# Optimization experiments

Hardware: AMD Instinct MI355X
Metric: run time of the kernel (lower is better)

## Reference

```python
import jax, jax.numpy as jnp
import numpy as np

N = 50000          # nodes
E = 800000         # edges (avg degree 16)
NS = 0.01          # LeakyReLU negative slope
N_CONVS = 3


def setup_inputs() -> dict:
    key = jax.random.key(0)
    ks = jax.random.split(key, 12)
    g = lambda k, s: (jax.random.normal(k, s, dtype=jnp.float32) * 0.05)
    return dict(
        x=jax.random.normal(ks[0], (N, 16), dtype=jnp.float32),
        edge_index=jax.random.randint(ks[1], (2, E), 0, N),
        edge_weight=jax.random.uniform(ks[2], (E, 1), dtype=jnp.float32),
        # prep MLP: Linear(16,64)+LeakyReLU, Linear(64,64)+Tanh
        Wp_in=g(ks[3], (16, 64)), bp_in=jnp.zeros((64,), jnp.float32),
        Wp_h=g(ks[4], (64, 64)), bp_h=jnp.zeros((64,), jnp.float32),
        # per-conv edge projection Linear(edge_dim=1, 64), stacked over 3 convs
        We=g(ks[5], (N_CONVS, 1, 64)), be=jnp.zeros((N_CONVS, 64), jnp.float32),
        # per-conv nn MLP: Linear(64,64)+LeakyReLU, Linear(64,64)+Tanh
        Wm0=g(ks[6], (N_CONVS, 64, 64)), bm0=jnp.zeros((N_CONVS, 64), jnp.float32),
        Wm1=g(ks[7], (N_CONVS, 64, 64)), bm1=jnp.zeros((N_CONVS, 64), jnp.float32),
        # post MLP: Linear(64,64)+LeakyReLU, Linear(64,32)+Tanh
        Wq0=g(ks[8], (64, 64)), bq0=jnp.zeros((64,), jnp.float32),
        Wq1=g(ks[9], (64, 32)), bq1=jnp.zeros((32,), jnp.float32),
    )


def reference(x, edge_index, edge_weight,
              Wp_in, bp_in, Wp_h, bp_h,
              We, be, Wm0, bm0, Wm1, bm1,
              Wq0, bq0, Wq1, bq1):
    lrelu = lambda v: jax.nn.leaky_relu(v, NS)
    # prep MLP (dropout=0 -> no-op)
    h = lrelu(x @ Wp_in + bp_in)
    h = jnp.tanh(h @ Wp_h + bp_h)
    src, dst = edge_index[0], edge_index[1]
    # stacked GINEConv layers (eps=0): out = nn(x + sum_j ReLU(x_j + lin_e(e_ij)))
    for k in range(N_CONVS):
        e = edge_weight @ We[k] + be[k]              # [E,64] edge embedding
        msg = jax.nn.relu(h[src] + e)                # [E,64] gather + fuse
        agg = jax.ops.segment_sum(msg, dst, num_segments=N)  # [N,64] scatter-sum
        z = agg + h                                  # (1+eps)*x with eps=0
        z = lrelu(z @ Wm0[k] + bm0[k])
        h = jnp.tanh(z @ Wm1[k] + bm1[k])
    # post MLP
    z = lrelu(h @ Wq0 + bq0)
    return jnp.tanh(z @ Wq1 + bq1)                   # [N,32]
```

## Files before the change

kernel.cpp:

```cpp
#include <hip/hip_runtime.h>
#include <hip/hip_fp16.h>
#include <math.h>

#define NS 0.01f
#define CAP 48
#define QS (1.f / 65535.f)

__device__ __forceinline__ float lrelu(float v) { return fmaxf(v, NS * v); }

__global__ void __launch_bounds__(512) build_kernel(
    const int* __restrict__ src, const int* __restrict__ dst,
    const float* __restrict__ ew, int* __restrict__ cnt,
    unsigned* __restrict__ bucket, int E, int fillBlocks,
    const float* __restrict__ x,
    const float* __restrict__ Wp_in, const float* __restrict__ bp_in,
    const float* __restrict__ Wp_h,  const float* __restrict__ bp_h,
    __half* __restrict__ h, int N, int prepBlocks,
    const float* __restrict__ Wm0, const float* __restrict__ Wm1,
    const float* __restrict__ Wq0, const float* __restrict__ Wq1,
    float* __restrict__ WT)
{
    __shared__ float zt[64 * 65];
    const int b = (int)blockIdx.x;
    const int t = threadIdx.x;

    if (b < fillBlocks) {
        const int e = b * 512 + t;
        if (e < E) {
            const int d = dst[e];
            const int p = atomicAdd(&cnt[d], 1);
            if (p < CAP) {
                const unsigned q = __float2uint_rn(ew[e] * 65535.f) & 0xffffu;
                bucket[(size_t)d * CAP + p] = ((unsigned)src[e] << 16) | q;
            }
        }
        return;
    }
    if (b < fillBlocks + prepBlocks) {
        const int n0 = (b - fillBlocks) * 64;
        #pragma unroll
        for (int r = 0; r < 2; ++r) {
            const int idx = r * 512 + t;
            const int nl = idx >> 4, i = idx & 15;
            const int n = n0 + nl;
            zt[nl * 65 + i] = (n < N) ? x[(size_t)n * 16 + i] : 0.f;
        }
        __syncthreads();
        const int lane = t & 63;
        const int w = __builtin_amdgcn_readfirstlane(t >> 6);
        float zx[16];
        #pragma unroll
        for (int i = 0; i < 16; ++i) zx[i] = zt[lane * 65 + i];
        float y[8];
        #pragma unroll
        for (int jj = 0; jj < 8; ++jj) {
            const int j = w * 8 + jj;
            float a = bp_in[j];
            #pragma unroll
            for (int i = 0; i < 16; ++i) a = fmaf(zx[i], Wp_in[i * 64 + j], a);
            y[jj] = lrelu(a);
        }
        __syncthreads();
        #pragma unroll
        for (int jj = 0; jj < 8; ++jj) zt[lane * 65 + w * 8 + jj] = y[jj];
        __syncthreads();
        #pragma unroll
        for (int jj = 0; jj < 8; ++jj) y[jj] = bp_h[w * 8 + jj];
        #pragma unroll
        for (int half = 0; half < 2; ++half) {
            float zh[32];
            #pragma unroll
            for (int i = 0; i < 32; ++i) zh[i] = zt[lane * 65 + half * 32 + i];
            #pragma unroll
            for (int jj = 0; jj < 8; ++jj) {
                const int j = w * 8 + jj;
                #pragma unroll
                for (int i = 0; i < 32; ++i)
                    y[jj] = fmaf(zh[i], Wp_h[(half * 32 + i) * 64 + j], y[jj]);
            }
        }
        __syncthreads();
        #pragma unroll
        for (int jj = 0; jj < 8; ++jj) zt[lane * 65 + w * 8 + jj] = tanhf(y[jj]);
        __syncthreads();
        #pragma unroll
        for (int r = 0; r < 8; ++r) {
            const int idx = r * 512 + t;
            const int nl = idx >> 6, i = idx & 63;
            const int n = n0 + nl;
            if (n < N) h[(size_t)n * 64 + i] = __float2half(zt[nl * 65 + i]);
        }
        return;
    }
    const int o = (b - fillBlocks - prepBlocks) * 512 + t;
    if (o >= 30720) return;
    float v;
    int d = o;
    if (d < 12288) {
        const int k = d >> 12, r = d & 4095, j = r >> 6, i = r & 63;
        v = Wm0[k * 4096 + i * 64 + j];
    } else if ((d -= 12288) < 12288) {
        const int k = d >> 12, r = d & 4095, j = r >> 6, i = r & 63;
        v = Wm1[k * 4096 + i * 64 + j];
    } else if ((d -= 12288) < 4096) {
        const int j = d >> 6, i = d & 63;
        v = Wq0[i * 64 + j];
    } else {
        d -= 4096;
        const int j = d >> 6, i = d & 63;
        v = Wq1[i * 32 + j];
    }
    WT[o] = v;
}

__device__ __forceinline__ void drain_edges(float& acc, int p, int len,
    const unsigned* row,
    const __half* __restrict__ hin, int lane, float wej, float bej)
{
    if (p + 4 <= len) {
        const uint4 a = ((const uint4*)row)[p >> 2];
        const unsigned r[4] = {a.x, a.y, a.z, a.w};
        float g[4];
        #pragma unroll
        for (int q = 0; q < 4; ++q) g[q] = __half2float(hin[(size_t)(r[q] >> 16) * 64 + lane]);
        #pragma unroll
        for (int q = 0; q < 4; ++q)
            acc += fmaxf(g[q] + fmaf((float)(r[q] & 0xffffu) * QS, wej, bej), 0.f);
        p += 4;
    }
    for (; p < len; ++p) {
        const unsigned r = row[p];
        acc += fmaxf(__half2float(hin[(size_t)(r >> 16) * 64 + lane])
                     + fmaf((float)(r & 0xffffu) * QS, wej, bej), 0.f);
    }
}

__device__ __forceinline__ void layer64s(float* zt, int lane, int w,
                                         const float* __restrict__ WT,
                                         const float* __restrict__ bias, int act)
{
    float y[4];
    #pragma unroll
    for (int jj = 0; jj < 4; ++jj) y[jj] = bias[w * 4 + jj];
    #pragma unroll
    for (int half = 0; half < 2; ++half) {
        float zh[32];
        #pragma unroll
        for (int i = 0; i < 32; ++i) zh[i] = zt[lane * 65 + half * 32 + i];
        #pragma unroll
        for (int jj = 0; jj < 4; ++jj) {
            const float* wr = WT + (w * 4 + jj) * 64 + half * 32;
            #pragma unroll
            for (int i = 0; i < 32; ++i) y[jj] = fmaf(zh[i], wr[i], y[jj]);
        }
    }
    __syncthreads();
    #pragma unroll
    for (int jj = 0; jj < 4; ++jj)
        zt[lane * 65 + w * 4 + jj] = act ? lrelu(y[jj]) : tanhf(y[jj]);
    __syncthreads();
}

__global__ void __launch_bounds__(1024, 8) fused_conv_kernel(
    const __half* __restrict__ hin,
    const int* __restrict__ cnt,
    const unsigned* __restrict__ bucket,
    const float* __restrict__ We_k, const float* __restrict__ be_k,
    const float* __restrict__ W0T, const float* __restrict__ b0,
    const float* __restrict__ W1T, const float* __restrict__ b1,
    const float* __restrict__ Wq0T, const float* __restrict__ bq0,
    const float* __restrict__ Wq1T, const float* __restrict__ bq1,
    int do_post, __half* __restrict__ hout, float* __restrict__ out, int N)
{
    __shared__ float zt[64 * 65];
    const int t = threadIdx.x;
    const int lane = t & 63;
    const int w = __builtin_amdgcn_readfirstlane(t >> 6);
    const int n0 = (int)blockIdx.x * 64;
    const float wej = We_k[lane], bej = be_k[lane];

    float acc[4];
    int   len[4];
    const unsigned* row[4];
    #pragma unroll
    for (int s = 0; s < 4; ++s) {
        const int n = n0 + w * 4 + s;
        if (n < N) { acc[s] = __half2float(hin[(size_t)n * 64 + lane]); len[s] = min(cnt[n], CAP); }
        else       { acc[s] = 0.f; len[s] = 0; }
        row[s] = bucket + (size_t)n * CAP;
    }
    const int maxLen = max(max(len[0], len[1]), max(len[2], len[3]));
    for (int p = 0; p + 8 <= maxLen; p += 8) {
        #pragma unroll
        for (int s = 0; s < 4; ++s) {
            if (p + 8 <= len[s]) {
                const uint4* r4 = (const uint4*)row[s];
                const uint4 a0 = r4[p >> 2], a1 = r4[(p >> 2) + 1];
                const unsigned rr[8] = {a0.x, a0.y, a0.z, a0.w, a1.x, a1.y, a1.z, a1.w};
                float g[8];
                #pragma unroll
                for (int q = 0; q < 8; ++q)
                    g[q] = __half2float(hin[(size_t)(rr[q] >> 16) * 64 + lane]);
                #pragma unroll
                for (int q = 0; q < 8; ++q)
                    acc[s] += fmaxf(g[q] + fmaf((float)(rr[q] & 0xffffu) * QS, wej, bej), 0.f);
            }
        }
    }
    #pragma unroll
    for (int s = 0; s < 4; ++s) {
        drain_edges(acc[s], len[s] & ~7, len[s], row[s], hin, lane, wej, bej);
        zt[(w * 4 + s) * 65 + lane] = acc[s];
    }
    __syncthreads();

    layer64s(zt, lane, w, W0T, b0, 1);
    layer64s(zt, lane, w, W1T, b1, 0);

    if (!do_post) {
        #pragma unroll
        for (int r = 0; r < 4; ++r) {
            const int idx = r * 1024 + t;
            const int nl = idx >> 6, i = idx & 63;
            const int n = n0 + nl;
            if (n < N) hout[(size_t)n * 64 + i] = __float2half(zt[nl * 65 + i]);
        }
        return;
    }
    layer64s(zt, lane, w, Wq0T, bq0, 1);
    {
        float y[2];
        #pragma unroll
        for (int jj = 0; jj < 2; ++jj) y[jj] = bq1[w * 2 + jj];
        #pragma unroll
        for (int half = 0; half < 2; ++half) {
            float zh[32];
            #pragma unroll
            for (int i = 0; i < 32; ++i) zh[i] = zt[lane * 65 + half * 32 + i];
            #pragma unroll
            for (int jj = 0; jj < 2; ++jj) {
                const float* wr = Wq1T + (w * 2 + jj) * 64 + half * 32;
                #pragma unroll
                for (int i = 0; i < 32; ++i) y[jj] = fmaf(zh[i], wr[i], y[jj]);
            }
        }
        __syncthreads();
        #pragma unroll
        for (int jj = 0; jj < 2; ++jj) zt[lane * 65 + w * 2 + jj] = tanhf(y[jj]);
        __syncthreads();
    }
    #pragma unroll
    for (int r = 0; r < 2; ++r) {
        const int idx = r * 1024 + t;
        const int nl = idx >> 5, i = idx & 31;
        const int n = n0 + nl;
        if (n < N) out[(size_t)n * 32 + i] = zt[nl * 65 + i];
    }
}

extern "C" void kernel_launch(void* const* d_in, const int* in_sizes, int n_in,
                              void* d_out, int out_size, void* d_ws, size_t ws_size,
                              hipStream_t stream) {
    const float* x     = (const float*)d_in[0];
    const int*   ei    = (const int*)d_in[1];
    const float* ew    = (const float*)d_in[2];
    const float* Wp_in = (const float*)d_in[3];
    const float* bp_in = (const float*)d_in[4];
    const float* Wp_h  = (const float*)d_in[5];
    const float* bp_h  = (const float*)d_in[6];
    const float* We    = (const float*)d_in[7];
    const float* be    = (const float*)d_in[8];
    const float* Wm0   = (const float*)d_in[9];
    const float* bm0   = (const float*)d_in[10];
    const float* Wm1   = (const float*)d_in[11];
    const float* bm1   = (const float*)d_in[12];
    const float* Wq0   = (const float*)d_in[13];
    const float* bq0   = (const float*)d_in[14];
    const float* Wq1   = (const float*)d_in[15];
    const float* bq1   = (const float*)d_in[16];
    float* out = (float*)d_out;

    const int N = in_sizes[0] / 16;
    const int E = in_sizes[2];
    const int* src = ei;
    const int* dst = ei + E;

    __half*   hA     = (__half*)d_ws;
    __half*   hB     = hA + (size_t)N * 64;
    unsigned* bucket = (unsigned*)(hB + (size_t)N * 64);
    int*      cnt    = (int*)(bucket + (size_t)N * CAP);
    float*    WT     = (float*)(cnt + N);
    float* Wm0T   = WT;
    float* Wm1T   = Wm0T + 12288;
    float* Wq0T   = Wm1T + 12288;
    float* Wq1T   = Wq0T + 4096;

    const int fillBlocks = (E + 511) / 512;
    const int prepBlocks = (N + 63) / 64;
    const int wtBlocks   = (30720 + 511) / 512;
    const int tileBlocks = (N + 63) / 64;

    hipMemsetAsync(cnt, 0, (size_t)N * sizeof(int), stream);
    build_kernel<<<fillBlocks + prepBlocks + wtBlocks, 512, 0, stream>>>(
        src, dst, ew, cnt, bucket, E, fillBlocks,
        x, Wp_in, bp_in, Wp_h, bp_h, hA, N, prepBlocks,
        Wm0, Wm1, Wq0, Wq1, WT);

    fused_conv_kernel<<<tileBlocks, 1024, 0, stream>>>(
        hA, cnt, bucket, We + 0 * 64, be + 0 * 64,
        Wm0T + 0 * 4096, bm0 + 0 * 64, Wm1T + 0 * 4096, bm1 + 0 * 64,
        Wq0T, bq0, Wq1T, bq1, 0, hB, out, N);
    fused_conv_kernel<<<tileBlocks, 1024, 0, stream>>>(
        hB, cnt, bucket, We + 1 * 64, be + 1 * 64,
        Wm0T + 1 * 4096, bm0 + 1 * 64, Wm1T + 1 * 4096, bm1 + 1 * 64,
        Wq0T, bq0, Wq1T, bq1, 0, hA, out, N);
    fused_conv_kernel<<<tileBlocks, 1024, 0, stream>>>(
        hA, cnt, bucket, We + 2 * 64, be + 2 * 64,
        Wm0T + 2 * 4096, bm0 + 2 * 64, Wm1T + 2 * 4096, bm1 + 2 * 64,
        Wq0T, bq0, Wq1T, bq1, 1, hB, out, N);
}
```

Baseline: 298.5 us.

## Fuse three conv launches into one persistent cooperative kernel with grid sync

Replaces the three per-layer conv kernel launches with a single cooperative persistent kernel. It loops over layers, processes node tiles in a grid-stride loop, and separates layers with a grid-wide sync while swapping the ping-pong buffers. The goal is to remove launch gaps and per-launch tail effects. In exchange it adds grid-sync overhead and an occupancy-limited grid size (hard-coded for 256 CUs), and each block must now loop over several tiles.

```diff
diff --git a/kernel.cpp b/kernel.cpp
--- a/kernel.cpp
+++ b/kernel.cpp
@@ -1,6 +1,9 @@
 #include <hip/hip_runtime.h>
+#include <hip/hip_cooperative_groups.h>
 #include <hip/hip_fp16.h>
 #include <math.h>
+
+namespace cg = cooperative_groups;
 
 #define NS 0.01f
 #define CAP 48
@@ -161,100 +164,118 @@
     __syncthreads();
 }
 
-__global__ void __launch_bounds__(1024, 8) fused_conv_kernel(
-    const __half* __restrict__ hin,
+__global__ void __launch_bounds__(1024, 8) conv3_kernel(
+    __half* __restrict__ hA, __half* __restrict__ hB,
     const int* __restrict__ cnt,
     const unsigned* __restrict__ bucket,
-    const float* __restrict__ We_k, const float* __restrict__ be_k,
-    const float* __restrict__ W0T, const float* __restrict__ b0,
-    const float* __restrict__ W1T, const float* __restrict__ b1,
+    const float* __restrict__ We, const float* __restrict__ be,
+    const float* __restrict__ Wm0T, const float* __restrict__ bm0,
+    const float* __restrict__ Wm1T, const float* __restrict__ bm1,
     const float* __restrict__ Wq0T, const float* __restrict__ bq0,
     const float* __restrict__ Wq1T, const float* __restrict__ bq1,
-    int do_post, __half* __restrict__ hout, float* __restrict__ out, int N)
+    float* __restrict__ out, int N, int tiles)
 {
+    cg::grid_group gridg = cg::this_grid();
     __shared__ float zt[64 * 65];
     const int t = threadIdx.x;
     const int lane = t & 63;
     const int w = __builtin_amdgcn_readfirstlane(t >> 6);
-    const int n0 = (int)blockIdx.x * 64;
-    const float wej = We_k[lane], bej = be_k[lane];
-
-    float acc[4];
-    int   len[4];
-    const unsigned* row[4];
-    #pragma unroll
-    for (int s = 0; s < 4; ++s) {
-        const int n = n0 + w * 4 + s;
-        if (n < N) { acc[s] = __half2float(hin[(size_t)n * 64 + lane]); len[s] = min(cnt[n], CAP); }
-        else       { acc[s] = 0.f; len[s] = 0; }
-        row[s] = bucket + (size_t)n * CAP;
-    }
-    const int maxLen = max(max(len[0], len[1]), max(len[2], len[3]));
-    for (int p = 0; p + 8 <= maxLen; p += 8) {
-        #pragma unroll
-        for (int s = 0; s < 4; ++s) {
-            if (p + 8 <= len[s]) {
-                const uint4* r4 = (const uint4*)row[s];
-                const uint4 a0 = r4[p >> 2], a1 = r4[(p >> 2) + 1];
-                const unsigned rr[8] = {a0.x, a0.y, a0.z, a0.w, a1.x, a1.y, a1.z, a1.w};
-                float g[8];
+
+    const __half* hin = hA;
+    __half* hout = hB;
+    for (int k = 0; k < 3; ++k) {
+        const float wej = We[k * 64 + lane], bej = be[k * 64 + lane];
+        const float* W0T = Wm0T + k * 4096; const float* b0 = bm0 + k * 64;
+        const float* W1T = Wm1T + k * 4096; const float* b1 = bm1 + k * 64;
+        const int do_post = (k == 2);
+
+        for (int tile = (int)blockIdx.x; tile < tiles; tile += (int)gridDim.x) {
+            const int n0 = tile * 64;
+
+            float acc[4];
+            int   len[4];
+            const unsigned* row[4];
+            #pragma unroll
+            for (int s = 0; s < 4; ++s) {
+                const int n = n0 + w * 4 + s;
+                if (n < N) { acc[s] = __half2float(hin[(size_t)n * 64 + lane]); len[s] = min(cnt[n], CAP); }
+                else       { acc[s] = 0.f; len[s] = 0; }
+                row[s] = bucket + (size_t)n * CAP;
+            }
+            const int maxLen = max(max(len[0], len[1]), max(len[2], len[3]));
+            for (int p = 0; p + 8 <= maxLen; p += 8) {
                 #pragma unroll
-                for (int q = 0; q < 8; ++q)
-                    g[q] = __half2float(hin[(size_t)(rr[q] >> 16) * 64 + lane]);
+                for (int s = 0; s < 4; ++s) {
+                    if (p + 8 <= len[s]) {
+                        const uint4* r4 = (const uint4*)row[s];
+                        const uint4 a0 = r4[p >> 2], a1 = r4[(p >> 2) + 1];
+                        const unsigned rr[8] = {a0.x, a0.y, a0.z, a0.w, a1.x, a1.y, a1.z, a1.w};
+                        float g[8];
+                        #pragma unroll
+                        for (int q = 0; q < 8; ++q)
+                            g[q] = __half2float(hin[(size_t)(rr[q] >> 16) * 64 + lane]);
+                        #pragma unroll
+                        for (int q = 0; q < 8; ++q)
+                            acc[s] += fmaxf(g[q] + fmaf((float)(rr[q] & 0xffffu) * QS, wej, bej), 0.f);
+                    }
+                }
+            }
+            #pragma unroll
+            for (int s = 0; s < 4; ++s) {
+                drain_edges(acc[s], len[s] & ~7, len[s], row[s], hin, lane, wej, bej);
+                zt[(w * 4 + s) * 65 + lane] = acc[s];
+            }
+            __syncthreads();
+
+            layer64s(zt, lane, w, W0T, b0, 1);
+            layer64s(zt, lane, w, W1T, b1, 0);
+
+            if (!do_post) {
                 #pragma unroll
-                for (int q = 0; q < 8; ++q)
-                    acc[s] += fmaxf(g[q] + fmaf((float)(rr[q] & 0xffffu) * QS, wej, bej), 0.f);
-            }
-        }
-    }
-    #pragma unroll
-    for (int s = 0; s < 4; ++s) {
-        drain_edges(acc[s], len[s] & ~7, len[s], row[s], hin, lane, wej, bej);
-        zt[(w * 4 + s) * 65 + lane] = acc[s];
-    }
-    __syncthreads();
-
-    layer64s(zt, lane, w, W0T, b0, 1);
-    layer64s(zt, lane, w, W1T, b1, 0);
-
-    if (!do_post) {
-        #pragma unroll
-        for (int r = 0; r < 4; ++r) {
-            const int idx = r * 1024 + t;
-            const int nl = idx >> 6, i = idx & 63;
-            const int n = n0 + nl;
-            if (n < N) hout[(size_t)n * 64 + i] = __float2half(zt[nl * 65 + i]);
-        }
-        return;
-    }
-    layer64s(zt, lane, w, Wq0T, bq0, 1);
-    {
-        float y[2];
-        #pragma unroll
-        for (int jj = 0; jj < 2; ++jj) y[jj] = bq1[w * 2 + jj];
-        #pragma unroll
-        for (int half = 0; half < 2; ++half) {
-            float zh[32];
-            #pragma unroll
-            for (int i = 0; i < 32; ++i) zh[i] = zt[lane * 65 + half * 32 + i];
-            #pragma unroll
-            for (int jj = 0; jj < 2; ++jj) {
-                const float* wr = Wq1T + (w * 2 + jj) * 64 + half * 32;
+                for (int r = 0; r < 4; ++r) {
+                    const int idx = r * 1024 + t;
+                    const int nl = idx >> 6, i = idx & 63;
+                    const int n = n0 + nl;
+                    if (n < N) hout[(size_t)n * 64 + i] = __float2half(zt[nl * 65 + i]);
+                }
+                __syncthreads();
+            } else {
+                layer64s(zt, lane, w, Wq0T, bq0, 1);
+                {
+                    float y[2];
+                    #pragma unroll
+                    for (int jj = 0; jj < 2; ++jj) y[jj] = bq1[w * 2 + jj];
+                    #pragma unroll
+                    for (int half = 0; half < 2; ++half) {
+                        float zh[32];
+                        #pragma unroll
+                        for (int i = 0; i < 32; ++i) zh[i] = zt[lane * 65 + half * 32 + i];
+                        #pragma unroll
+                        for (int jj = 0; jj < 2; ++jj) {
+                            const float* wr = Wq1T + (w * 2 + jj) * 64 + half * 32;
+                            #pragma unroll
+                            for (int i = 0; i < 32; ++i) y[jj] = fmaf(zh[i], wr[i], y[jj]);
+                        }
+                    }
+                    __syncthreads();
+                    #pragma unroll
+                    for (int jj = 0; jj < 2; ++jj) zt[lane * 65 + w * 2 + jj] = tanhf(y[jj]);
+                    __syncthreads();
+                }
                 #pragma unroll
-                for (int i = 0; i < 32; ++i) y[jj] = fmaf(zh[i], wr[i], y[jj]);
-            }
-        }
-        __syncthreads();
-        #pragma unroll
-        for (int jj = 0; jj < 2; ++jj) zt[lane * 65 + w * 2 + jj] = tanhf(y[jj]);
-        __syncthreads();
-    }
-    #pragma unroll
-    for (int r = 0; r < 2; ++r) {
-        const int idx = r * 1024 + t;
-        const int nl = idx >> 5, i = idx & 31;
-        const int n = n0 + nl;
-        if (n < N) out[(size_t)n * 32 + i] = zt[nl * 65 + i];
+                for (int r = 0; r < 2; ++r) {
+                    const int idx = r * 1024 + t;
+                    const int nl = idx >> 5, i = idx & 31;
+                    const int n = n0 + nl;
+                    if (n < N) out[(size_t)n * 32 + i] = zt[nl * 65 + i];
+                }
+                __syncthreads();
+            }
+        }
+        if (k < 2) {
+            gridg.sync();
+            const __half* tmp = hin; hin = hout; hout = (__half*)tmp;
+        }
     }
 }
 
@@ -306,16 +327,19 @@
         x, Wp_in, bp_in, Wp_h, bp_h, hA, N, prepBlocks,
         Wm0, Wm1, Wq0, Wq1, WT);
 
-    fused_conv_kernel<<<tileBlocks, 1024, 0, stream>>>(
-        hA, cnt, bucket, We + 0 * 64, be + 0 * 64,
-        Wm0T + 0 * 4096, bm0 + 0 * 64, Wm1T + 0 * 4096, bm1 + 0 * 64,
-        Wq0T, bq0, Wq1T, bq1, 0, hB, out, N);
-    fused_conv_kernel<<<tileBlocks, 1024, 0, stream>>>(
-        hB, cnt, bucket, We + 1 * 64, be + 1 * 64,
-        Wm0T + 1 * 4096, bm0 + 1 * 64, Wm1T + 1 * 4096, bm1 + 1 * 64,
-        Wq0T, bq0, Wq1T, bq1, 0, hA, out, N);
-    fused_conv_kernel<<<tileBlocks, 1024, 0, stream>>>(
-        hA, cnt, bucket, We + 2 * 64, be + 2 * 64,
-        Wm0T + 2 * 4096, bm0 + 2 * 64, Wm1T + 2 * 4096, bm1 + 2 * 64,
-        Wq0T, bq0, Wq1T, bq1, 1, hB, out, N);
-}
+    int occ = 0;
+    hipOccupancyMaxActiveBlocksPerMultiprocessor(&occ, (const void*)conv3_kernel, 1024, 0);
+    if (occ < 1) occ = 1;
+    int grid = occ * 256;
+    if (grid > tileBlocks) grid = tileBlocks;
+
+    void* args[] = {
+        (void*)&hA, (void*)&hB, (void*)&cnt, (void*)&bucket,
+        (void*)&We, (void*)&be,
+        (void*)&Wm0T, (void*)&bm0, (void*)&Wm1T, (void*)&bm1,
+        (void*)&Wq0T, (void*)&bq0, (void*)&Wq1T, (void*)&bq1,
+        (void*)&out, (void*)&N, (void*)&tileBlocks
+    };
+    hipLaunchCooperativeKernel((void*)conv3_kernel, dim3(grid), dim3(1024),
+                               args, 0, stream);
+}
```

Result: slower. 683.6 us (+129.1%).
